# Kernel optimization log

Hardware: AMD Instinct MI355X
Metric: run time of the kernel (lower is better)

Reference implementation:

```python
import jax, jax.numpy as jnp
import numpy as np

EMBED_DIM = 256
HEADS = 8
HEAD_DIM = EMBED_DIM // HEADS
T = 8            # time grid points
N0, N1 = 32, 32  # spatial grid
MAX_PATCH = 16   # static slot budget per cell (last slot = grid latent token)
NEG = -1e30


def construct_grid():
    g0 = jnp.linspace(0.0, 1.0, N0)
    g1 = jnp.linspace(0.0, 1.0, N1)
    G0, G1 = jnp.meshgrid(g0, g1, indexing='ij')
    return jnp.stack([G0, G1], axis=-1)  # [N0, N1, 2]


def setup_inputs() -> dict:
    key = jax.random.key(0)
    ks = jax.random.split(key, 8)
    m, n = 4, 16384
    x = jax.random.uniform(ks[0], (m, n, 3))                       # coords: (time, s0, s1) in [0,1]
    z = jax.random.normal(ks[1], (m, n, EMBED_DIM))
    time_grid = jnp.tile(jnp.linspace(0.0, 1.0, T)[None], (m, 1))  # [m, T] uniform time grid
    latents = jax.random.normal(ks[2], (N0, N1, EMBED_DIM))
    grid = construct_grid()
    s = 1.0 / np.sqrt(EMBED_DIM)
    Wq = jax.random.normal(ks[3], (EMBED_DIM, EMBED_DIM)) * s
    Wk = jax.random.normal(ks[4], (EMBED_DIM, EMBED_DIM)) * s
    Wv = jax.random.normal(ks[5], (EMBED_DIM, EMBED_DIM)) * s
    Wo = jax.random.normal(ks[6], (EMBED_DIM, EMBED_DIM)) * s
    return {'x': x, 'z': z, 'time_grid': time_grid, 'latents': latents,
            'grid': grid, 'Wq': Wq, 'Wk': Wk, 'Wv': Wv, 'Wo': Wo}


def _cumcount(idx):
    # idx: [n] int; returns per-element count of prior occurrences of the same value
    n = idx.shape[0]
    order = jnp.argsort(idx)                 # stable
    srt = idx[order]
    ar = jnp.arange(n)
    is_start = jnp.concatenate([jnp.array([True]), srt[1:] != srt[:-1]])
    seg_start = jax.lax.cummax(jnp.where(is_start, ar, 0), axis=0)
    cc = ar - seg_start
    return jnp.zeros_like(idx).at[order].set(cc.astype(idx.dtype))


def _forward(x, z, time_grid, latents, grid, Wq, Wk, Wv, Wo):
    m, n, _ = x.shape
    t = time_grid.shape[1]
    S = t * N0 * N1
    # --- build x_grid: repeat spatial grid over (m,t), insert time coord at dim 0 ---
    xg_sp = jnp.broadcast_to(grid[None, None], (m, t, N0, N1, 2))
    tg = jnp.broadcast_to(time_grid[:, :, None, None, None], (m, t, N0, N1, 1))
    x_grid = jnp.concatenate([tg, xg_sp], axis=-1)          # [m,t,N0,N1,3]
    # --- nearest gridded neighbour (k=1): per-dim rounding on the regular grid ---
    grid_shape = jnp.array([t, N0, N1], jnp.float32)
    xg_flat = x_grid.reshape(m, S, 3)
    xmin = xg_flat.min(axis=1)                               # [m,3]
    xmax = xg_flat.max(axis=1)
    spacing = (xmax - xmin) / (grid_shape - 1.0)             # [m,3]
    multi = jnp.floor((x - xmin[:, None] + spacing[:, None] / 2) / spacing[:, None])
    multi = jnp.clip(multi, 0.0, grid_shape - 1.0)
    strides = jnp.array([N0 * N1, N1, 1], jnp.float32)
    nearest = jnp.sum(multi * strides, axis=-1).astype(jnp.int32)  # [m,n] flat cell id
    # --- per-cell slot allocation via cumulative count ---
    cum = jax.vmap(_cumcount)(nearest)                       # [m,n]
    P = MAX_PATCH
    valid = cum < (P - 1)                                    # last slot reserved for grid token
    bidx = jnp.arange(m)[:, None]
    cell = jnp.where(valid, nearest, S)                      # out-of-bounds -> dropped
    slot = jnp.minimum(cum, P - 2)
    # --- scatter points into the joint grid [m, S, P, E]; slot P-1 = grid latent ---
    joint = jnp.zeros((m, S, P, EMBED_DIM), z.dtype)
    joint = joint.at[bidx, cell, slot].set(z, mode='drop')
    z_grid_flat = jnp.broadcast_to(
        latents.reshape(1, 1, N0 * N1, EMBED_DIM), (m, t, N0 * N1, EMBED_DIM)
    ).reshape(m, S, EMBED_DIM)
    joint = joint.at[:, :, P - 1].set(z_grid_flat)
    counts = jnp.zeros((m, S), jnp.int32).at[bidx, cell].add(1, mode='drop')
    counts = jnp.minimum(counts, P - 1)
    att_mask = jnp.concatenate(
        [jnp.arange(P - 1)[None, None] < counts[..., None],
         jnp.ones((m, S, 1), bool)], axis=-1)                # [m,S,P]
    # --- masked multi-head cross attention: 1 query (grid latent) per cell ---
    q = (z_grid_flat @ Wq).reshape(m, S, HEADS, HEAD_DIM)
    k = (joint @ Wk).reshape(m, S, P, HEADS, HEAD_DIM)
    v = (joint @ Wv).reshape(m, S, P, HEADS, HEAD_DIM)
    logits = jnp.einsum('mshd,msphd->mshp', q, k) / np.sqrt(HEAD_DIM)
    logits = jnp.where(att_mask[:, :, None, :], logits, NEG)
    attn = jax.nn.softmax(logits, axis=-1)
    out = jnp.einsum('mshp,msphd->mshd', attn, v).reshape(m, S, EMBED_DIM) @ Wo
    z_grid = out.reshape(m, t, N0, N1, EMBED_DIM)
    return x_grid, z_grid


def reference(x, z, time_grid, latents, grid, Wq, Wk, Wv, Wo):
    return _forward(x, z, time_grid, latents, grid, Wq, Wk, Wv, Wo)
```

## Files before the change

kernel.cpp:

```cpp
#include <hip/hip_runtime.h>
#include <hip/hip_bf16.h>

#define T_ 8
#define N0_ 32
#define N1_ 32
#define SP_ (N0_*N1_)
#define S_ (T_*SP_)
#define E_ 256
#define P_ 16
#define NH_ 8
#define HD_ 32

typedef __attribute__((ext_vector_type(8))) short short8;
typedef __attribute__((ext_vector_type(4))) float f32x4;
typedef __attribute__((ext_vector_type(8))) unsigned short u16x8;

__device__ __forceinline__ unsigned short f2bf(float f) {
  __hip_bfloat16 h = __float2bfloat16(f);
  return *reinterpret_cast<unsigned short*>(&h);
}
__device__ __forceinline__ float bf2f(unsigned short u) {
  return __uint_as_float((unsigned)u << 16);
}

__device__ __forceinline__ void gl_lds16(const void* g, void* l) {
  __builtin_amdgcn_global_load_lds(
      (const __attribute__((address_space(1))) unsigned int*)(g),
      (__attribute__((address_space(3))) unsigned int*)(l), 16, 0, 0);
}

__global__ __launch_bounds__(256) void prep(const float* __restrict__ z,
                                            unsigned short* __restrict__ z16,
                                            const float* __restrict__ x,
                                            const float* __restrict__ tg,
                                            const float* __restrict__ grid,
                                            float* __restrict__ out,
                                            int* __restrict__ counts,
                                            int* __restrict__ cell_raw,
                                            const float* __restrict__ Wq,
                                            const float* __restrict__ Wk,
                                            const float* __restrict__ Wv,
                                            const float* __restrict__ Wo,
                                            unsigned short* __restrict__ wT,
                                            const float* __restrict__ latents,
                                            unsigned short* __restrict__ lat16,
                                            int m, int n, int tot_xg, int zn8) {
  __shared__ float ts[64][65];
  __shared__ float st[4][6];
  int bid = blockIdx.x;
  int tid = threadIdx.x;
  if (bid < 2048) {
    for (int i = bid * 256 + tid; i < zn8; i += 2048 * 256) {
      float4 a = *(const float4*)(z + (size_t)i * 8);
      float4 b = *(const float4*)(z + (size_t)i * 8 + 4);
      u16x8 o;
      o[0]=f2bf(a.x); o[1]=f2bf(a.y); o[2]=f2bf(a.z); o[3]=f2bf(a.w);
      o[4]=f2bf(b.x); o[5]=f2bf(b.y); o[6]=f2bf(b.z); o[7]=f2bf(b.w);
      *(u16x8*)(z16 + (size_t)i * 8) = o;
    }
    return;
  }
  if (bid < 2304) {
    if (tid < 64) {
      float mn0 = 1e30f, mx0 = -1e30f, mn1 = 1e30f, mx1 = -1e30f;
      for (int i = tid; i < SP_; i += 64) {
        float g0 = grid[i*2], g1 = grid[i*2+1];
        mn0 = fminf(mn0, g0); mx0 = fmaxf(mx0, g0);
        mn1 = fminf(mn1, g1); mx1 = fmaxf(mx1, g1);
      }
      for (int msk = 32; msk; msk >>= 1) {
        mn0 = fminf(mn0, __shfl_xor(mn0, msk));
        mx0 = fmaxf(mx0, __shfl_xor(mx0, msk));
        mn1 = fminf(mn1, __shfl_xor(mn1, msk));
        mx1 = fmaxf(mx1, __shfl_xor(mx1, msk));
      }
      if (tid == 0) {
        for (int b = 0; b < m; ++b) {
          float tmn = 1e30f, tmx = -1e30f;
          for (int tt = 0; tt < T_; ++tt) {
            float v = tg[b*T_ + tt];
            tmn = fminf(tmn, v); tmx = fmaxf(tmx, v);
          }
          st[b][0] = tmn; st[b][1] = mn0; st[b][2] = mn1;
          st[b][3] = (tmx - tmn) / (float)(T_ - 1);
          st[b][4] = (mx0 - mn0) / (float)(N0_ - 1);
          st[b][5] = (mx1 - mn1) / (float)(N1_ - 1);
        }
      }
    }
    __syncthreads();
    int idx = (bid - 2048) * 256 + tid;
    if (idx < tot_xg) {
      int sp = idx & (SP_ - 1);
      int bt = idx >> 10;
      out[idx*3 + 0] = tg[bt];
      out[idx*3 + 1] = grid[sp*2 + 0];
      out[idx*3 + 2] = grid[sp*2 + 1];
    }
    if (idx < m*n) {
      int b = idx / n;
      int j = idx - b*n;
      const float* s = st[b];
      float xt = x[(size_t)idx*3 + 0], x0 = x[(size_t)idx*3 + 1], x1 = x[(size_t)idx*3 + 2];
      float m0 = floorf((xt - s[0] + s[3]*0.5f) / s[3]);
      float m1 = floorf((x0 - s[1] + s[4]*0.5f) / s[4]);
      float m2 = floorf((x1 - s[2] + s[5]*0.5f) / s[5]);
      m0 = fminf(fmaxf(m0, 0.f), (float)(T_ - 1));
      m1 = fminf(fmaxf(m1, 0.f), (float)(N0_ - 1));
      m2 = fminf(fmaxf(m2, 0.f), (float)(N1_ - 1));
      int sc = (int)m0 * SP_ + (int)m1 * N1_ + (int)m2;
      int cg = b * S_ + sc;
      int old = atomicAdd(&counts[cg], 1);
      if (old < P_) cell_raw[(size_t)cg * P_ + old] = j;
    }
    return;
  }
  if (bid < 2368) {
    int wb = bid - 2304;
    int mat = wb >> 4;
    int tile = wb & 15;
    int tr = (tile >> 2) * 64;
    int tc = (tile & 3) * 64;
    const float* W = mat == 0 ? Wq : mat == 1 ? Wk : mat == 2 ? Wv : Wo;
    int r = tid >> 2, c0 = (tid & 3) * 16;
#pragma unroll
    for (int i = 0; i < 4; ++i) {
      float4 v = *(const float4*)&W[(size_t)(tr + r) * 256 + tc + c0 + i*4];
      ts[r][c0 + i*4 + 0] = v.x; ts[r][c0 + i*4 + 1] = v.y;
      ts[r][c0 + i*4 + 2] = v.z; ts[r][c0 + i*4 + 3] = v.w;
    }
    __syncthreads();
    u16x8 o0, o1;
#pragma unroll
    for (int i = 0; i < 8; ++i) o0[i] = f2bf(ts[c0 + i][r]);
#pragma unroll
    for (int i = 0; i < 8; ++i) o1[i] = f2bf(ts[c0 + 8 + i][r]);
    unsigned short* dst = wT + (size_t)(mat * 256 + tc + r) * 256 + tr + c0;
    *(u16x8*)dst = o0;
    *(u16x8*)(dst + 8) = o1;
    return;
  }
  for (int i = (bid - 2368) * 256 + tid; i < SP_ * E_ / 8; i += 16 * 256) {
    float4 a = *(const float4*)(latents + (size_t)i * 8);
    float4 b = *(const float4*)(latents + (size_t)i * 8 + 4);
    u16x8 o;
    o[0]=f2bf(a.x); o[1]=f2bf(a.y); o[2]=f2bf(a.z); o[3]=f2bf(a.w);
    o[4]=f2bf(b.x); o[5]=f2bf(b.y); o[6]=f2bf(b.z); o[7]=f2bf(b.w);
    *(u16x8*)(lat16 + (size_t)i * 8) = o;
  }
}

template <typename OutT>
__device__ __forceinline__ void g2l_body(unsigned short* __restrict__ ldsbuf,
                                         const unsigned short* __restrict__ A,
                                         const unsigned short* __restrict__ BT,
                                         OutT* __restrict__ C,
                                         int CP, int ldc, int L, int tid) {
  int rp = L / CP, cp = L - rp * CP;

  int wid = tid >> 6, lane = tid & 63, l15 = lane & 15, slot = lane >> 4;
  int wr = (wid >> 1) * 64, wc = (wid & 1) * 64;

  int r8 = lane >> 3, k8 = lane & 7;
  int colsw = (k8 ^ r8) << 3;
  const unsigned short* ga0 = A  + (size_t)(rp * 128 + wid * 32 + r8) * 256 + colsw;
  const unsigned short* gb0 = BT + (size_t)(cp * 128 + wid * 32 + r8) * 256 + colsw;

#define STAGE(b, kt) do { \
    const unsigned short* ga = ga0 + (kt) * 64; \
    const unsigned short* gb = gb0 + (kt) * 64; \
    gl_lds16(ga,          ldsbuf + ((b)*2    ) * 8192 + (wid*32     ) * 64); \
    gl_lds16(ga +  8*256, ldsbuf + ((b)*2    ) * 8192 + (wid*32 +  8) * 64); \
    gl_lds16(ga + 16*256, ldsbuf + ((b)*2    ) * 8192 + (wid*32 + 16) * 64); \
    gl_lds16(ga + 24*256, ldsbuf + ((b)*2    ) * 8192 + (wid*32 + 24) * 64); \
    gl_lds16(gb,          ldsbuf + ((b)*2 + 1) * 8192 + (wid*32     ) * 64); \
    gl_lds16(gb +  8*256, ldsbuf + ((b)*2 + 1) * 8192 + (wid*32 +  8) * 64); \
    gl_lds16(gb + 16*256, ldsbuf + ((b)*2 + 1) * 8192 + (wid*32 + 16) * 64); \
    gl_lds16(gb + 24*256, ldsbuf + ((b)*2 + 1) * 8192 + (wid*32 + 24) * 64); \
  } while (0)

  f32x4 acc[4][4] = {};
  STAGE(0, 0);

#pragma unroll
  for (int kt = 0; kt < 4; ++kt) {
    int b = kt & 1;
    if (kt < 3) STAGE(b ^ 1, kt + 1);
    if (kt < 3) asm volatile("s_waitcnt vmcnt(8)" ::: "memory");
    else        asm volatile("s_waitcnt vmcnt(0)" ::: "memory");
    __builtin_amdgcn_s_barrier();
    asm volatile("" ::: "memory");
    const unsigned short* As = ldsbuf + (b*2) * 8192;
    const unsigned short* Bs = ldsbuf + (b*2 + 1) * 8192;
#pragma unroll
    for (int kf = 0; kf < 2; ++kf) {
      short8 afr[4], bfr[4];
      int sx = (kf * 4 + slot) ^ (l15 & 7);
#pragma unroll
      for (int mm = 0; mm < 4; ++mm) {
        int row = wr + mm * 16 + l15;
        afr[mm] = *(const short8*)&As[row * 64 + (sx << 3)];
      }
#pragma unroll
      for (int nn = 0; nn < 4; ++nn) {
        int col = wc + nn * 16 + l15;
        bfr[nn] = *(const short8*)&Bs[col * 64 + (sx << 3)];
      }
#pragma unroll
      for (int mm = 0; mm < 4; ++mm)
#pragma unroll
        for (int nn = 0; nn < 4; ++nn)
          acc[mm][nn] = __builtin_amdgcn_mfma_f32_16x16x32_bf16(afr[mm], bfr[nn], acc[mm][nn], 0, 0, 0);
    }
    asm volatile("" ::: "memory");
    __builtin_amdgcn_s_barrier();
    asm volatile("" ::: "memory");
  }
#undef STAGE

#pragma unroll
  for (int mm = 0; mm < 4; ++mm) {
#pragma unroll
    for (int nn = 0; nn < 4; ++nn) {
      int grow0 = rp * 128 + wr + mm * 16 + slot * 4;
      int gcol  = cp * 128 + wc + nn * 16 + l15;
#pragma unroll
      for (int j = 0; j < 4; ++j) {
        size_t o = (size_t)(grow0 + j) * ldc + gcol;
        if constexpr (__is_same(OutT, float)) C[o] = acc[mm][nn][j];
        else                                  C[o] = __float2bfloat16(acc[mm][nn][j]);
      }
    }
  }
}

__global__ __launch_bounds__(256, 2) void phase2(const unsigned short* __restrict__ z16,
                                                 const unsigned short* __restrict__ wT,
                                                 __hip_bfloat16* __restrict__ kv,
                                                 const unsigned short* __restrict__ lat16,
                                                 float* __restrict__ lat,
                                                 const int* __restrict__ counts,
                                                 int* __restrict__ cell_raw,
                                                 int* __restrict__ pts2, int total) {
  __shared__ unsigned short lds[4 * 128 * 64];
  int bid = blockIdx.x;
  if (bid < 2048) {
    int L = (bid & 7) * 256 + (bid >> 3);
    g2l_body<__hip_bfloat16>(lds, z16, wT + (size_t)256*256, kv, 4, 512, L, threadIdx.x);
    return;
  }
  if (bid < 2096) {
    g2l_body<float>(lds, lat16, wT, lat, 6, 768, bid - 2048, threadIdx.x);
    return;
  }
  int cg = (bid - 2096) * 256 + threadIdx.x;
  if (cg >= total) return;
  int cnt = counts[cg];
  int stored = cnt < P_ ? cnt : P_;
  int eff = cnt < (P_ - 1) ? cnt : (P_ - 1);
  int* p = cell_raw + (size_t)cg * P_;
  for (int i = 1; i < stored; ++i) {
    int key = p[i]; int j = i - 1;
    while (j >= 0 && p[j] > key) { p[j+1] = p[j]; --j; }
    p[j+1] = key;
  }
  int* o = pts2 + (size_t)cg * P_;
  o[0] = eff;
  for (int i = 0; i < eff; ++i) o[1 + i] = p[i];
}

template <typename OutT>
__global__ __launch_bounds__(256, 2) void gemm_g2l(const unsigned short* __restrict__ A,
                                                   const unsigned short* __restrict__ BT,
                                                   OutT* __restrict__ C,
                                                   int CP, int ldc) {
  __shared__ unsigned short lds[4 * 128 * 64];
  int nb = gridDim.x, bid = blockIdx.x;
  int L = bid;
  if ((nb & 7) == 0) L = (bid & 7) * (nb >> 3) + (bid >> 3);
  g2l_body<OutT>(lds, A, BT, C, CP, ldc, L, threadIdx.x);
}

__global__ __launch_bounds__(256) void attn_kernel(
    const float* __restrict__ lat,
    const __hip_bfloat16* __restrict__ kv,
    const int* __restrict__ pts2,
    __hip_bfloat16* __restrict__ attn_out, int n) {
  const float scale = 0.17677669529663687f;
  int wid = threadIdx.x >> 6;
  int lane = threadIdx.x & 63;
  int cellg = blockIdx.x * 4 + wid;
  int b = cellg >> 13;
  int c = cellg & (SP_ - 1);
  int d0 = lane << 2;

  const int* pp = pts2 + (size_t)cellg * P_;
  int4 h0 = *(const int4*)pp;
  int eff = h0.x;

  const float* latc = lat + c * 768 + d0;
  float4 q  = *(const float4*)latc;
  float4 kl = *(const float4*)(latc + 256);
  float4 vl = *(const float4*)(latc + 512);

  float p15 = q.x*kl.x + q.y*kl.y + q.z*kl.z + q.w*kl.w;
  p15 += __shfl_xor(p15, 1);
  p15 += __shfl_xor(p15, 2);
  p15 += __shfl_xor(p15, 4);
  float e15 = __expf(p15 * scale);
  float ssum = e15;
  float4 acc;
  acc.x = e15 * vl.x; acc.y = e15 * vl.y; acc.z = e15 * vl.z; acc.w = e15 * vl.w;

  const unsigned short* kvp = (const unsigned short*)kv;
  size_t bbase = (size_t)b * n;

  int pt[4]; pt[0] = h0.y; pt[1] = h0.z; pt[2] = h0.w; pt[3] = 0;
  int done = 0, cap = 3;
  while (done < eff) {
    int np = eff - done; if (np > cap) np = cap;
    ushort4 kr[4], vr[4];
#pragma unroll
    for (int i = 0; i < 4; ++i) if (i < np) {
      size_t row = (bbase + (size_t)pt[i]) * 512;
      kr[i] = *(const ushort4*)(kvp + row + d0);
      vr[i] = *(const ushort4*)(kvp + row + 256 + d0);
    }
    float e[4];
#pragma unroll
    for (int i = 0; i < 4; ++i) if (i < np) {
      float p = q.x*bf2f(kr[i].x) + q.y*bf2f(kr[i].y) + q.z*bf2f(kr[i].z) + q.w*bf2f(kr[i].w);
      p += __shfl_xor(p, 1);
      p += __shfl_xor(p, 2);
      p += __shfl_xor(p, 4);
      e[i] = __expf(p * scale);
    }
#pragma unroll
    for (int i = 0; i < 4; ++i) if (i < np) {
      ssum += e[i];
      acc.x += e[i] * bf2f(vr[i].x);
      acc.y += e[i] * bf2f(vr[i].y);
      acc.z += e[i] * bf2f(vr[i].z);
      acc.w += e[i] * bf2f(vr[i].w);
    }
    done += np;
    cap = 4;
    if (done < eff) {
      int4 h = *(const int4*)(pp + 1 + done);
      pt[0] = h.x; pt[1] = h.y; pt[2] = h.z; pt[3] = h.w;
    }
  }
  float inv = 1.f / ssum;
  ushort4 o;
  o.x = f2bf(acc.x * inv); o.y = f2bf(acc.y * inv);
  o.z = f2bf(acc.z * inv); o.w = f2bf(acc.w * inv);
  *(ushort4*)((unsigned short*)attn_out + (size_t)cellg * E_ + d0) = o;
}

extern "C" void kernel_launch(void* const* d_in, const int* in_sizes, int n_in,
                              void* d_out, int out_size, void* d_ws, size_t ws_size,
                              hipStream_t stream) {
  const float* x       = (const float*)d_in[0];
  const float* z       = (const float*)d_in[1];
  const float* tg      = (const float*)d_in[2];
  const float* latents = (const float*)d_in[3];
  const float* grid    = (const float*)d_in[4];
  const float* Wq      = (const float*)d_in[5];
  const float* Wk      = (const float*)d_in[6];
  const float* Wv      = (const float*)d_in[7];
  const float* Wo      = (const float*)d_in[8];

  int m = in_sizes[2] / T_;
  int n = in_sizes[1] / (m * E_);
  int MS = m * S_;
  float* out = (float*)d_out;
  int tot_xg = m * T_ * SP_;

  char* w = (char*)d_ws;
  auto alloc = [&](size_t bytes) { char* p = w; w += (bytes + 255) & ~(size_t)255; return p; };
  int*   counts     = (int*)  alloc((size_t)MS * 4);
  int*   cell_raw   = (int*)  alloc((size_t)MS * P_ * 4);
  int*   pts2       = (int*)  alloc((size_t)MS * P_ * 4);
  unsigned short* wT    = (unsigned short*)alloc((size_t)1024 * 256 * 2);
  unsigned short* lat16 = (unsigned short*)alloc((size_t)SP_ * E_ * 2);
  float* lat        = (float*)alloc((size_t)SP_ * 768 * 4);
  __hip_bfloat16* kv       = (__hip_bfloat16*)alloc((size_t)m * n * 512 * 2);
  __hip_bfloat16* attn_out = (__hip_bfloat16*)alloc((size_t)MS * E_ * 2);

  unsigned short* z16 = (unsigned short*)(out + (size_t)tot_xg * 3);

  (void)hipMemsetAsync(counts, 0, (size_t)MS * 4, stream);

  prep<<<2384, 256, 0, stream>>>(z, z16, x, tg, grid, out, counts, cell_raw,
                                 Wq, Wk, Wv, Wo, wT, latents, lat16,
                                 m, n, tot_xg, m * n * E_ / 8);

  phase2<<<2224, 256, 0, stream>>>(z16, wT, kv, lat16, lat, counts, cell_raw, pts2, MS);

  attn_kernel<<<MS/4, 256, 0, stream>>>(lat, kv, pts2, attn_out, n);

  gemm_g2l<float><<<512, 256, 0, stream>>>(
      (const unsigned short*)attn_out, wT + (size_t)768*256, out + (size_t)tot_xg * 3, 2, 256);
}
```

Measured before the change: 92.34 us.

## Fold Wk into per-head query and apply Wv after attention to skip K/V projection

Instead of projecting all z tokens through Wk and Wv into a large bf16 K/V buffer, the query is premultiplied by the per-head slice of Wk, giving a per-cell, per-head vector in embedding space. Attention scores are then dot products with raw fp32 z rows. The softmax-weighted mix of z is formed per head and multiplied by Wv with MFMA inside a fused attention kernel. This removes the big z→bf16 conversion and the K/V GEMM over all points, in exchange for more per-cell work (8 heads × full 256-dim reductions with extra shuffles) and an extra small GEMM producing the qm table.

```diff
diff --git a/kernel.cpp b/kernel.cpp
--- a/kernel.cpp
+++ b/kernel.cpp
@@ -29,38 +29,25 @@
       (__attribute__((address_space(3))) unsigned int*)(l), 16, 0, 0);
 }
 
-__global__ __launch_bounds__(256) void prep(const float* __restrict__ z,
-                                            unsigned short* __restrict__ z16,
-                                            const float* __restrict__ x,
-                                            const float* __restrict__ tg,
-                                            const float* __restrict__ grid,
-                                            float* __restrict__ out,
-                                            int* __restrict__ counts,
-                                            int* __restrict__ cell_raw,
-                                            const float* __restrict__ Wq,
-                                            const float* __restrict__ Wk,
-                                            const float* __restrict__ Wv,
-                                            const float* __restrict__ Wo,
-                                            unsigned short* __restrict__ wT,
-                                            const float* __restrict__ latents,
-                                            unsigned short* __restrict__ lat16,
-                                            int m, int n, int tot_xg, int zn8) {
+__global__ __launch_bounds__(256) void prep1(const float* __restrict__ x,
+                                             const float* __restrict__ tg,
+                                             const float* __restrict__ grid,
+                                             float* __restrict__ out,
+                                             int* __restrict__ counts,
+                                             int* __restrict__ cell_raw,
+                                             const float* __restrict__ Wq,
+                                             const float* __restrict__ Wk,
+                                             const float* __restrict__ Wv,
+                                             const float* __restrict__ Wo,
+                                             unsigned short* __restrict__ wT,
+                                             const float* __restrict__ latents,
+                                             unsigned short* __restrict__ lat16,
+                                             int m, int n, int tot_xg) {
   __shared__ float ts[64][65];
   __shared__ float st[4][6];
   int bid = blockIdx.x;
   int tid = threadIdx.x;
-  if (bid < 2048) {
-    for (int i = bid * 256 + tid; i < zn8; i += 2048 * 256) {
-      float4 a = *(const float4*)(z + (size_t)i * 8);
-      float4 b = *(const float4*)(z + (size_t)i * 8 + 4);
-      u16x8 o;
-      o[0]=f2bf(a.x); o[1]=f2bf(a.y); o[2]=f2bf(a.z); o[3]=f2bf(a.w);
-      o[4]=f2bf(b.x); o[5]=f2bf(b.y); o[6]=f2bf(b.z); o[7]=f2bf(b.w);
-      *(u16x8*)(z16 + (size_t)i * 8) = o;
-    }
-    return;
-  }
-  if (bid < 2304) {
+  if (bid < 256) {
     if (tid < 64) {
       float mn0 = 1e30f, mx0 = -1e30f, mn1 = 1e30f, mx1 = -1e30f;
       for (int i = tid; i < SP_; i += 64) {
@@ -89,7 +76,7 @@
       }
     }
     __syncthreads();
-    int idx = (bid - 2048) * 256 + tid;
+    int idx = bid * 256 + tid;
     if (idx < tot_xg) {
       int sp = idx & (SP_ - 1);
       int bt = idx >> 10;
@@ -115,8 +102,8 @@
     }
     return;
   }
-  if (bid < 2368) {
-    int wb = bid - 2304;
+  if (bid < 320) {
+    int wb = bid - 256;
     int mat = wb >> 4;
     int tile = wb & 15;
     int tr = (tile >> 2) * 64;
@@ -140,7 +127,7 @@
     *(u16x8*)(dst + 8) = o1;
     return;
   }
-  for (int i = (bid - 2368) * 256 + tid; i < SP_ * E_ / 8; i += 16 * 256) {
+  for (int i = (bid - 320) * 256 + tid; i < SP_ * E_ / 8; i += 16 * 256) {
     float4 a = *(const float4*)(latents + (size_t)i * 8);
     float4 b = *(const float4*)(latents + (size_t)i * 8 + 4);
     u16x8 o;
@@ -234,26 +221,37 @@
   }
 }
 
-__global__ __launch_bounds__(256, 2) void phase2(const unsigned short* __restrict__ z16,
-                                                 const unsigned short* __restrict__ wT,
-                                                 __hip_bfloat16* __restrict__ kv,
-                                                 const unsigned short* __restrict__ lat16,
-                                                 float* __restrict__ lat,
-                                                 const int* __restrict__ counts,
-                                                 int* __restrict__ cell_raw,
-                                                 int* __restrict__ pts2, int total) {
+__global__ __launch_bounds__(256, 2) void prep2(const unsigned short* __restrict__ lat16,
+                                                const unsigned short* __restrict__ wT,
+                                                __hip_bfloat16* __restrict__ q16,
+                                                unsigned short* __restrict__ Bqm,
+                                                const int* __restrict__ counts,
+                                                int* __restrict__ cell_raw,
+                                                int* __restrict__ pts2, int total) {
   __shared__ unsigned short lds[4 * 128 * 64];
-  int bid = blockIdx.x;
-  if (bid < 2048) {
-    int L = (bid & 7) * 256 + (bid >> 3);
-    g2l_body<__hip_bfloat16>(lds, z16, wT + (size_t)256*256, kv, 4, 512, L, threadIdx.x);
+  int bid = blockIdx.x, tid = threadIdx.x;
+  if (bid < 16) {
+    g2l_body<__hip_bfloat16>(lds, lat16, wT, q16, 2, 256, bid, tid);
     return;
   }
-  if (bid < 2096) {
-    g2l_body<float>(lds, lat16, wT, lat, 6, 768, bid - 2048, threadIdx.x);
+  if (bid < 48) {
+    int r = (bid - 16) * 64 + (tid >> 2);
+    int h = r >> 8, d = r & 255;
+    int fq = (tid & 3) * 64;
+    const unsigned short* wTk = wT + 256 * 256;
+    unsigned short* dst = Bqm + (size_t)r * 256 + fq;
+    for (int i = 0; i < 64; i += 8) {
+      u16x8 v;
+#pragma unroll
+      for (int j = 0; j < 8; ++j) {
+        int f = fq + i + j;
+        v[j] = (f >> 5) == h ? wTk[(size_t)((h << 5) + (f & 31)) * 256 + d] : (unsigned short)0;
+      }
+      *(u16x8*)(dst + i) = v;
+    }
     return;
   }
-  int cg = (bid - 2096) * 256 + threadIdx.x;
+  int cg = (bid - 48) * 256 + tid;
   if (cg >= total) return;
   int cnt = counts[cg];
   int stored = cnt < P_ ? cnt : P_;
@@ -281,80 +279,114 @@
   g2l_body<OutT>(lds, A, BT, C, CP, ldc, L, threadIdx.x);
 }
 
-__global__ __launch_bounds__(256) void attn_kernel(
-    const float* __restrict__ lat,
-    const __hip_bfloat16* __restrict__ kv,
-    const int* __restrict__ pts2,
-    __hip_bfloat16* __restrict__ attn_out, int n) {
+__global__ __launch_bounds__(256, 2) void mega_attn(const float* __restrict__ z,
+                                                    const float* __restrict__ latents,
+                                                    const float* __restrict__ qm,
+                                                    const unsigned short* __restrict__ wTv,
+                                                    const int* __restrict__ pts2,
+                                                    __hip_bfloat16* __restrict__ attn_out,
+                                                    int n) {
+  __shared__ unsigned short mixlds[16 * 2048];
   const float scale = 0.17677669529663687f;
-  int wid = threadIdx.x >> 6;
-  int lane = threadIdx.x & 63;
-  int cellg = blockIdx.x * 4 + wid;
-  int b = cellg >> 13;
-  int c = cellg & (SP_ - 1);
+  int tid = threadIdx.x, w = tid >> 6, lane = tid & 63;
   int d0 = lane << 2;
-
-  const int* pp = pts2 + (size_t)cellg * P_;
-  int4 h0 = *(const int4*)pp;
-  int eff = h0.x;
-
-  const float* latc = lat + c * 768 + d0;
-  float4 q  = *(const float4*)latc;
-  float4 kl = *(const float4*)(latc + 256);
-  float4 vl = *(const float4*)(latc + 512);
-
-  float p15 = q.x*kl.x + q.y*kl.y + q.z*kl.z + q.w*kl.w;
-  p15 += __shfl_xor(p15, 1);
-  p15 += __shfl_xor(p15, 2);
-  p15 += __shfl_xor(p15, 4);
-  float e15 = __expf(p15 * scale);
-  float ssum = e15;
-  float4 acc;
-  acc.x = e15 * vl.x; acc.y = e15 * vl.y; acc.z = e15 * vl.z; acc.w = e15 * vl.w;
-
-  const unsigned short* kvp = (const unsigned short*)kv;
-  size_t bbase = (size_t)b * n;
-
-  int pt[4]; pt[0] = h0.y; pt[1] = h0.z; pt[2] = h0.w; pt[3] = 0;
-  int done = 0, cap = 3;
-  while (done < eff) {
-    int np = eff - done; if (np > cap) np = cap;
-    ushort4 kr[4], vr[4];
-#pragma unroll
-    for (int i = 0; i < 4; ++i) if (i < np) {
-      size_t row = (bbase + (size_t)pt[i]) * 512;
-      kr[i] = *(const ushort4*)(kvp + row + d0);
-      vr[i] = *(const ushort4*)(kvp + row + 256 + d0);
-    }
-    float e[4];
-#pragma unroll
-    for (int i = 0; i < 4; ++i) if (i < np) {
-      float p = q.x*bf2f(kr[i].x) + q.y*bf2f(kr[i].y) + q.z*bf2f(kr[i].z) + q.w*bf2f(kr[i].w);
-      p += __shfl_xor(p, 1);
-      p += __shfl_xor(p, 2);
-      p += __shfl_xor(p, 4);
-      e[i] = __expf(p * scale);
-    }
-#pragma unroll
-    for (int i = 0; i < 4; ++i) if (i < np) {
-      ssum += e[i];
-      acc.x += e[i] * bf2f(vr[i].x);
-      acc.y += e[i] * bf2f(vr[i].y);
-      acc.z += e[i] * bf2f(vr[i].z);
-      acc.w += e[i] * bf2f(vr[i].w);
-    }
-    done += np;
-    cap = 4;
-    if (done < eff) {
-      int4 h = *(const int4*)(pp + 1 + done);
-      pt[0] = h.x; pt[1] = h.y; pt[2] = h.z; pt[3] = h.w;
-    }
-  }
-  float inv = 1.f / ssum;
-  ushort4 o;
-  o.x = f2bf(acc.x * inv); o.y = f2bf(acc.y * inv);
-  o.z = f2bf(acc.z * inv); o.w = f2bf(acc.w * inv);
-  *(ushort4*)((unsigned short*)attn_out + (size_t)cellg * E_ + d0) = o;
+  int cg0 = blockIdx.x * 16;
+
+  for (int cc = 0; cc < 4; ++cc) {
+    int cellL = w * 4 + cc;
+    int cellg = cg0 + cellL;
+    int bidx = cellg >> 13;
+    int c = cellg & (SP_ - 1);
+
+    float4 qmr[8];
+#pragma unroll
+    for (int h = 0; h < 8; ++h)
+      qmr[h] = *(const float4*)(qm + (size_t)c * 2048 + h * 256 + d0);
+
+    const int* pp = pts2 + (size_t)cellg * P_;
+    int4 h0 = *(const int4*)pp;
+    int eff = h0.x;
+
+    float4 zl = *(const float4*)(latents + (size_t)c * 256 + d0);
+    float ss[8];
+    float mx[8][4];
+#pragma unroll
+    for (int h = 0; h < 8; ++h) {
+      float p = qmr[h].x*zl.x + qmr[h].y*zl.y + qmr[h].z*zl.z + qmr[h].w*zl.w;
+      p += __shfl_xor(p, 1);  p += __shfl_xor(p, 2);  p += __shfl_xor(p, 4);
+      p += __shfl_xor(p, 8);  p += __shfl_xor(p, 16); p += __shfl_xor(p, 32);
+      float e = __expf(p * scale);
+      ss[h] = e;
+      mx[h][0] = e*zl.x; mx[h][1] = e*zl.y; mx[h][2] = e*zl.z; mx[h][3] = e*zl.w;
+    }
+
+    size_t bb = (size_t)bidx * n;
+    int pt[4]; pt[0] = h0.y; pt[1] = h0.z; pt[2] = h0.w; pt[3] = 0;
+    int done = 0, cap = 3;
+    while (done < eff) {
+      int np = eff - done; if (np > cap) np = cap;
+      float4 zr[4];
+#pragma unroll
+      for (int i = 0; i < 4; ++i) if (i < np)
+        zr[i] = *(const float4*)(z + (bb + (size_t)pt[i]) * 256 + d0);
+#pragma unroll
+      for (int i = 0; i < 4; ++i) if (i < np) {
+#pragma unroll
+        for (int h = 0; h < 8; ++h) {
+          float p = qmr[h].x*zr[i].x + qmr[h].y*zr[i].y + qmr[h].z*zr[i].z + qmr[h].w*zr[i].w;
+          p += __shfl_xor(p, 1);  p += __shfl_xor(p, 2);  p += __shfl_xor(p, 4);
+          p += __shfl_xor(p, 8);  p += __shfl_xor(p, 16); p += __shfl_xor(p, 32);
+          float e = __expf(p * scale);
+          ss[h] += e;
+          mx[h][0] += e*zr[i].x; mx[h][1] += e*zr[i].y;
+          mx[h][2] += e*zr[i].z; mx[h][3] += e*zr[i].w;
+        }
+      }
+      done += np;
+      cap = 4;
+      if (done < eff) {
+        int4 hh = *(const int4*)(pp + 1 + done);
+        pt[0] = hh.x; pt[1] = hh.y; pt[2] = hh.z; pt[3] = hh.w;
+      }
+    }
+
+    unsigned base = (unsigned)cellL * 4096;
+    unsigned K = cellL & 7;
+#pragma unroll
+    for (int h = 0; h < 8; ++h) {
+      float inv = 1.f / ss[h];
+      unsigned g = (unsigned)(h * 32 + (lane >> 1));
+      unsigned addr = base + ((g ^ K) << 4) + ((unsigned)(d0 & 7) << 1);
+      ushort4 v;
+      v.x = f2bf(mx[h][0] * inv); v.y = f2bf(mx[h][1] * inv);
+      v.z = f2bf(mx[h][2] * inv); v.w = f2bf(mx[h][3] * inv);
+      *(ushort4*)((char*)mixlds + addr) = v;
+    }
+  }
+  __syncthreads();
+
+  int l15 = lane & 15, slot = lane >> 4;
+#pragma unroll
+  for (int hh = 0; hh < 2; ++hh) {
+    int h = w + hh * 4;
+    f32x4 acc0 = {}, acc1 = {};
+#pragma unroll
+    for (int ks = 0; ks < 8; ++ks) {
+      unsigned gA = (unsigned)(h * 32 + ks * 4 + slot);
+      short8 afr = *(const short8*)((const char*)mixlds + l15 * 4096 + ((gA ^ (unsigned)(l15 & 7)) << 4));
+      short8 b0 = *(const short8*)(wTv + (size_t)(h * 32 + l15) * 256 + ks * 32 + slot * 8);
+      short8 b1 = *(const short8*)(wTv + (size_t)(h * 32 + 16 + l15) * 256 + ks * 32 + slot * 8);
+      acc0 = __builtin_amdgcn_mfma_f32_16x16x32_bf16(afr, b0, acc0, 0, 0, 0);
+      acc1 = __builtin_amdgcn_mfma_f32_16x16x32_bf16(afr, b1, acc1, 0, 0, 0);
+    }
+    unsigned short* op = (unsigned short*)attn_out;
+#pragma unroll
+    for (int j = 0; j < 4; ++j) {
+      size_t row = (size_t)(cg0 + slot * 4 + j) * 256 + h * 32;
+      op[row + l15]      = f2bf(acc0[j]);
+      op[row + 16 + l15] = f2bf(acc1[j]);
+    }
+  }
 }
 
 extern "C" void kernel_launch(void* const* d_in, const int* in_sizes, int n_in,
@@ -383,21 +415,22 @@
   int*   pts2       = (int*)  alloc((size_t)MS * P_ * 4);
   unsigned short* wT    = (unsigned short*)alloc((size_t)1024 * 256 * 2);
   unsigned short* lat16 = (unsigned short*)alloc((size_t)SP_ * E_ * 2);
-  float* lat        = (float*)alloc((size_t)SP_ * 768 * 4);
-  __hip_bfloat16* kv       = (__hip_bfloat16*)alloc((size_t)m * n * 512 * 2);
+  __hip_bfloat16* q16   = (__hip_bfloat16*)alloc((size_t)SP_ * E_ * 2);
+  unsigned short* Bqm   = (unsigned short*)alloc((size_t)2048 * 256 * 2);
+  float* qm         = (float*)alloc((size_t)SP_ * 2048 * 4);
   __hip_bfloat16* attn_out = (__hip_bfloat16*)alloc((size_t)MS * E_ * 2);
 
-  unsigned short* z16 = (unsigned short*)(out + (size_t)tot_xg * 3);
-
   (void)hipMemsetAsync(counts, 0, (size_t)MS * 4, stream);
 
-  prep<<<2384, 256, 0, stream>>>(z, z16, x, tg, grid, out, counts, cell_raw,
-                                 Wq, Wk, Wv, Wo, wT, latents, lat16,
-                                 m, n, tot_xg, m * n * E_ / 8);
-
-  phase2<<<2224, 256, 0, stream>>>(z16, wT, kv, lat16, lat, counts, cell_raw, pts2, MS);
-
-  attn_kernel<<<MS/4, 256, 0, stream>>>(lat, kv, pts2, attn_out, n);
+  prep1<<<336, 256, 0, stream>>>(x, tg, grid, out, counts, cell_raw,
+                                 Wq, Wk, Wv, Wo, wT, latents, lat16, m, n, tot_xg);
+
+  prep2<<<176, 256, 0, stream>>>(lat16, wT, q16, Bqm, counts, cell_raw, pts2, MS);
+
+  gemm_g2l<float><<<128, 256, 0, stream>>>((const unsigned short*)q16, Bqm, qm, 16, 2048);
+
+  mega_attn<<<MS/16, 256, 0, stream>>>(z, latents, qm, wT + (size_t)2*256*256, pts2,
+                                       attn_out, n);
 
   gemm_g2l<float><<<512, 256, 0, stream>>>(
       (const unsigned short*)attn_out, wT + (size_t)768*256, out + (size_t)tot_xg * 3, 2, 256);
```

Result: slower. 169.2 us (+83.2%).
